# Kernel optimization log

Hardware: AMD Instinct MI355X
Metric: run time of the kernel (lower is better)

## Reference

```python
import jax, jax.numpy as jnp
import numpy as np

B, S, E = 2, 2049, 512
H, WIN = 8, 1024
D = E // H


def setup_inputs() -> dict:
    key = jax.random.key(0)
    ks = jax.random.split(key, 11)
    sc = 0.02
    return {
        "x": jax.random.normal(ks[0], (B, S, E), dtype=jnp.float32),
        "Wq": jax.random.normal(ks[1], (E, E), dtype=jnp.float32) * sc,
        "bq": jnp.zeros((E,), dtype=jnp.float32),
        "Wk": jax.random.normal(ks[2], (E, E), dtype=jnp.float32) * sc,
        "bk": jnp.zeros((E,), dtype=jnp.float32),
        "Wv": jax.random.normal(ks[3], (E, E), dtype=jnp.float32) * sc,
        "bv": jnp.zeros((E,), dtype=jnp.float32),
        "Wo": jax.random.normal(ks[4], (E, E), dtype=jnp.float32) * sc,
        "bo": jnp.zeros((E,), dtype=jnp.float32),
        "w_gate": jax.random.normal(ks[5], (2 * E,), dtype=jnp.float32) * sc,
        "b_gate": jnp.zeros((), dtype=jnp.float32),
    }


def reference(x, Wq, bq, Wk, bk, Wv, bv, Wo, bo, w_gate, b_gate):
    scale = D ** -0.5
    q_flat = x @ Wq + bq  # [B,S,E]
    k_flat = x @ Wk + bk
    v_flat = x @ Wv + bv
    q = q_flat.reshape(B, S, H, D).transpose(0, 2, 1, 3)  # [B,H,S,D]
    k = k_flat.reshape(B, S, H, D).transpose(0, 2, 1, 3)
    v = v_flat.reshape(B, S, H, D).transpose(0, 2, 1, 3)

    scores = jnp.einsum("bhqd,bhkd->bhqk", q, k) * scale  # [B,H,S,S]

    # Gaussian positional bias: -0.5*|i-j|^2/sigma^2, sigma = window/2
    pos = jnp.arange(S)
    dist = jnp.abs(pos[:, None] - pos[None, :]).astype(jnp.float32)
    sigma = WIN / 2.0
    bias = -0.5 * dist ** 2 / (sigma ** 2)  # [S,S]
    scores = scores + bias[None, None]

    # Pairwise gate: sigmoid(concat(q_i,k_j) @ w + b) == sigmoid(q_i.wq + k_j.wk + b)
    gq = q_flat @ w_gate[:E]       # [B,S]
    gk = k_flat @ w_gate[E:]       # [B,S]
    gates = jax.nn.sigmoid(gq[:, :, None] + gk[:, None, :] + b_gate)  # [B,S,S]
    scores = scores * gates[:, None]  # broadcast over heads

    local_mask = jnp.where(dist <= WIN, 0.0, -jnp.inf).astype(jnp.float32)
    scores = scores + local_mask[None, None]

    attn = jax.nn.softmax(scores, axis=-1)
    out = jnp.einsum("bhqk,bhkd->bhqd", attn, v)  # [B,H,S,D]
    out = out.transpose(0, 2, 1, 3).reshape(B, S, E)
    return out @ Wo + bo
```

## Files before the change

kernel.cpp:

```cpp
#include <hip/hip_runtime.h>
#include <cstdint>
#include <cstddef>

#define B_ 2
#define S_ 2049
#define E_ 512
#define H_ 8
#define WIN_ 1024
#define MROWS (B_*S_)
#define SP_ 2176
#define GBUFN 4104
#define BHS_ (B_*H_*S_)

typedef unsigned short ushort_t;
typedef __attribute__((ext_vector_type(8))) short bf16x8;
typedef __attribute__((ext_vector_type(4))) float f32x4;

#define MFMA16(a,b,c) __builtin_amdgcn_mfma_f32_16x16x32_bf16(a,b,c,0,0,0)

__device__ __forceinline__ ushort_t f2bf(float f) {
  unsigned int u = __float_as_uint(f);
  u += 0x7fffu + ((u >> 16) & 1u);
  return (ushort_t)(u >> 16);
}
__device__ __forceinline__ float bf2f(ushort_t h) {
  return __uint_as_float(((unsigned int)h) << 16);
}

__global__ __launch_bounds__(256) void convert_all_kernel(
    const float* __restrict__ x, const float* __restrict__ W0,
    const float* __restrict__ W1, const float* __restrict__ W2,
    const float* __restrict__ W3, ushort_t* __restrict__ xb,
    ushort_t* __restrict__ Wt_all, ushort_t* __restrict__ WoHi,
    float* __restrict__ gacc)
{
  __shared__ float tile[32][33];
  int bid = blockIdx.x;
  if (bid < 2049) {
    int idx = bid * 256 + threadIdx.x;
    float4 v = ((const float4*)x)[idx];
    ushort4 o;
    o.x = f2bf(v.x); o.y = f2bf(v.y); o.z = f2bf(v.z); o.w = f2bf(v.w);
    ((ushort4*)xb)[idx] = o;
    return;
  }
  int wid = bid - 2049;
  int z = wid >> 8, rem = wid & 255;
  if (z == 3) {
    int gz = rem * 256 + threadIdx.x;
    if (gz < 2 * GBUFN) gacc[gz] = 0.f;
  }
  const float* W = (z == 0) ? W0 : (z == 1) ? W1 : (z == 2) ? W2 : W3;
  int k0 = (rem >> 4) * 32, n0 = (rem & 15) * 32;
  int r = threadIdx.x >> 5, c = threadIdx.x & 31;
#pragma unroll
  for (int i = 0; i < 4; ++i) {
    int rr = r + i * 8;
    tile[rr][c] = W[(size_t)(k0 + rr) * E_ + n0 + c];
  }
  __syncthreads();
#pragma unroll
  for (int i = 0; i < 4; ++i) {
    int rr = r + i * 8;
    float v = tile[c][rr];
    size_t dst = (size_t)(n0 + rr) * E_ + k0 + c;
    if (z < 3) Wt_all[(size_t)z * E_ * E_ + dst] = f2bf(v);
    else       WoHi[dst] = f2bf(v);
  }
}

__global__ __launch_bounds__(256) void gemm_qkv_kernel(
    const ushort_t* __restrict__ xb, const ushort_t* __restrict__ Wt_all,
    const float* __restrict__ bq, const float* __restrict__ bk,
    const float* __restrict__ bv, const float* __restrict__ wg,
    ushort_t* __restrict__ qkb, ushort_t* __restrict__ vT,
    float* __restrict__ gacc)
{
  __shared__ __align__(16) ushort_t As[64][72];
  __shared__ __align__(16) ushort_t Bs[128][72];
  int tid = threadIdx.x;
  int lane = tid & 63, w = tid >> 6;
  int l15 = lane & 15, quad = lane >> 4;
  int wm = (w & 1) * 32, wn = (w >> 1) * 64;
  int z = blockIdx.z;
  const ushort_t* Wt = Wt_all + (size_t)z * E_ * E_;
  const float* bias = (z == 0) ? bq : (z == 1) ? bk : bv;
  int bt = blockIdx.x;
  int bg2 = bt / 33;
  int bm = (bt - bg2 * 33) * 64;
  int bn = blockIdx.y * 128;
  size_t rowbase = (size_t)bg2 * S_;

  int ar = tid >> 2, acq = (tid & 3) * 16;
  int ai = bm + ar; if (ai >= S_) ai = S_ - 1;
  const ushort_t* ap = xb + (rowbase + ai) * E_ + acq;
  int br = tid >> 1, bcq = (tid & 1) * 32;
  const ushort_t* bp = Wt + (size_t)(bn + br) * E_ + bcq;

  const f32x4 fz = {0.f, 0.f, 0.f, 0.f};
  f32x4 acc[2][4];
#pragma unroll
  for (int mt = 0; mt < 2; ++mt)
#pragma unroll
    for (int nt = 0; nt < 4; ++nt) acc[mt][nt] = fz;

  int4 pa0 = *(const int4*)ap, pa1 = *(const int4*)(ap + 8);
  int4 pb0 = *(const int4*)bp,        pb1 = *(const int4*)(bp + 8);
  int4 pb2 = *(const int4*)(bp + 16), pb3 = *(const int4*)(bp + 24);

  for (int k0 = 0; k0 < E_; k0 += 64) {
    __syncthreads();
    int kn = (k0 + 64 < E_) ? (k0 + 64) : k0;
    int4 na0 = *(const int4*)(ap + kn), na1 = *(const int4*)(ap + kn + 8);
    int4 nb0 = *(const int4*)(bp + kn),      nb1 = *(const int4*)(bp + kn + 8);
    int4 nb2 = *(const int4*)(bp + kn + 16), nb3 = *(const int4*)(bp + kn + 24);
    *(int4*)&As[ar][acq] = pa0; *(int4*)&As[ar][acq + 8] = pa1;
    *(int4*)&Bs[br][bcq] = pb0;      *(int4*)&Bs[br][bcq + 8] = pb1;
    *(int4*)&Bs[br][bcq + 16] = pb2; *(int4*)&Bs[br][bcq + 24] = pb3;
    __syncthreads();
    bf16x8 a[2][2], bfr[4][2];
#pragma unroll
    for (int mt = 0; mt < 2; ++mt) {
      a[mt][0] = *(const bf16x8*)&As[wm + mt * 16 + l15][quad * 8];
      a[mt][1] = *(const bf16x8*)&As[wm + mt * 16 + l15][32 + quad * 8];
    }
#pragma unroll
    for (int nt = 0; nt < 4; ++nt) {
      bfr[nt][0] = *(const bf16x8*)&Bs[wn + nt * 16 + l15][quad * 8];
      bfr[nt][1] = *(const bf16x8*)&Bs[wn + nt * 16 + l15][32 + quad * 8];
    }
    __builtin_amdgcn_s_setprio(1);
#pragma unroll
    for (int mt = 0; mt < 2; ++mt)
#pragma unroll
      for (int nt = 0; nt < 4; ++nt) {
        acc[mt][nt] = MFMA16(a[mt][0], bfr[nt][0], acc[mt][nt]);
        acc[mt][nt] = MFMA16(a[mt][1], bfr[nt][1], acc[mt][nt]);
      }
    __builtin_amdgcn_s_setprio(0);
    pa0 = na0; pa1 = na1; pb0 = nb0; pb1 = nb1; pb2 = nb2; pb3 = nb3;
  }

  float bb[4];
#pragma unroll
  for (int nt = 0; nt < 4; ++nt) bb[nt] = bias[bn + wn + nt * 16 + l15];

  if (z < 2) {
    ushort_t* C = qkb + (size_t)z * MROWS * E_;
#pragma unroll
    for (int mt = 0; mt < 2; ++mt)
#pragma unroll
      for (int nt = 0; nt < 4; ++nt)
#pragma unroll
        for (int r = 0; r < 4; ++r) {
          int i = bm + wm + mt * 16 + quad * 4 + r;
          if (i < S_)
            C[(rowbase + i) * E_ + bn + wn + nt * 16 + l15] = f2bf(acc[mt][nt][r] + bb[nt]);
        }
    const float* wgp = wg + (size_t)z * E_;
    float wv[4];
#pragma unroll
    for (int nt = 0; nt < 4; ++nt) wv[nt] = wgp[bn + wn + nt * 16 + l15];
    float* gp = gacc + (size_t)z * GBUFN;
#pragma unroll
    for (int mt = 0; mt < 2; ++mt)
#pragma unroll
      for (int r = 0; r < 4; ++r) {
        float s = 0.f;
#pragma unroll
        for (int nt = 0; nt < 4; ++nt) s = fmaf(acc[mt][nt][r] + bb[nt], wv[nt], s);
        s += __shfl_xor(s, 1, 16); s += __shfl_xor(s, 2, 16);
        s += __shfl_xor(s, 4, 16); s += __shfl_xor(s, 8, 16);
        int i = bm + wm + mt * 16 + quad * 4 + r;
        if (l15 == 0 && i < S_) atomicAdd(&gp[rowbase + i], s);
      }
  } else {
    ushort_t* lt = &Bs[0][0];
    int ti = tid >> 2, tc = (tid & 3) * 16;
#pragma unroll
    for (int hh = 0; hh < 2; ++hh) {
      __syncthreads();
      if ((w >> 1) == hh) {
#pragma unroll
        for (int mt = 0; mt < 2; ++mt)
#pragma unroll
          for (int nt = 0; nt < 4; ++nt) {
            int d = nt * 16 + l15;
#pragma unroll
            for (int r = 0; r < 4; ++r) {
              int il = wm + mt * 16 + quad * 4 + r;
              lt[d * 72 + il] = f2bf(acc[mt][nt][r] + bb[nt]);
            }
          }
      }
      __syncthreads();
      int hg = (bn >> 6) + hh;
      union { int4 q[2]; ushort_t u[16]; } tv;
      tv.q[0] = *(const int4*)&lt[ti * 72 + tc];
      tv.q[1] = *(const int4*)&lt[ti * 72 + tc + 8];
      size_t vrow = ((size_t)(bg2 * H_ + hg) * 64 + ti) * SP_;
#pragma unroll
      for (int c8 = 0; c8 < 2; ++c8) {
        int i2 = bm + tc + c8 * 8;
        if (i2 + 7 < S_) {
          *(int4*)&vT[vrow + i2] = tv.q[c8];
        } else {
#pragma unroll
          for (int e = 0; e < 8; ++e)
            if (i2 + e < S_) vT[vrow + i2 + e] = tv.u[c8 * 8 + e];
        }
      }
    }
  }
}

__global__ __launch_bounds__(256) void attn_kernel(
    const ushort_t* __restrict__ qb, const ushort_t* __restrict__ kb,
    const ushort_t* __restrict__ vT, const float* __restrict__ gq_raw,
    const float* __restrict__ gk_raw, const float* __restrict__ bgate,
    float* __restrict__ Opart, float* __restrict__ Lpart)
{
  __shared__ __align__(16) ushort_t Ks[64][72];
  __shared__ __align__(16) ushort_t Vt[64][72];
  __shared__ __align__(16) ushort_t Ps[4][16][72];
  __shared__ float gbs[704];

  int tid = threadIdx.x;
  int lane = tid & 63, w = tid >> 6;
  int l15 = lane & 15, quad = lane >> 4;

  int sub = blockIdx.x % 48;
  int qidx = blockIdx.x / 48;
  int off = (qidx + 1) >> 1;
  int qt = 16 + ((qidx & 1) ? -off : off);
  int bh = sub & 15, third = sub >> 4;
  int h = bh & 7, b = bh >> 3;
  int i0 = qt * 64;
  const float LOG2E = 1.44269504f;
  const float coef2 = (-0.5f / (512.f * 512.f)) * LOG2E;
  const float QSC = 0.125f * LOG2E;

  int i = i0 + w * 16 + l15;
  int ic = (i < S_) ? i : S_ - 1;
  bf16x8 qf0 = *(const bf16x8*)&qb[((size_t)(b * S_ + ic)) * E_ + h * 64 + quad * 8];
  bf16x8 qf1 = *(const bf16x8*)&qb[((size_t)(b * S_ + ic)) * E_ + h * 64 + 32 + quad * 8];
#pragma unroll
  for (int e = 0; e < 8; ++e) {
    qf0[e] = (short)f2bf(bf2f((ushort_t)qf0[e]) * QSC);
    qf1[e] = (short)f2bf(bf2f((ushort_t)qf1[e]) * QSC);
  }
  float av = __expf(-(gq_raw[b * S_ + ic] + bgate[0]));
  float fdi = (i < S_) ? (float)i : -1e5f;

  int jlo = i0 - WIN_; if (jlo < 0) jlo = 0;
  int jt_lo = jlo >> 6;
  int jhi = i0 + 63 + WIN_; if (jhi > S_ - 1) jhi = S_ - 1;
  int jt_hi = jhi >> 6;
  int L = jt_hi - jt_lo + 1;
  int n0 = (L + 2) / 3, n1 = (L + 1) / 3;
  int myLo = jt_lo + ((third == 0) ? 0 : (third == 1) ? n0 : n0 + n1);
  int cnt = (third == 0) ? n0 : (third == 1) ? n1 : L - n0 - n1;
  int myHi = myLo + cnt - 1;
  int jbase = myLo << 6;
  int nwin = cnt << 6;

  for (int tt = tid; tt < nwin; tt += 256) {
    int j = jbase + tt; int jc = (j < S_) ? j : S_ - 1;
    gbs[tt] = __expf(-gk_raw[b * S_ + jc]);
  }

  int srow = tid >> 2, scol = (tid & 3) * 16;
  const ushort_t* kb_base = kb + (size_t)b * S_ * E_ + h * 64 + scol;
  const ushort_t* vb_base = vT + ((size_t)(b * H_ + h) * 64 + srow) * SP_ + scol;

  int4 ka0, ka1, va0, va1;
  {
    int jc0 = jbase + srow; if (jc0 > S_ - 1) jc0 = S_ - 1;
    const int4* kp = (const int4*)(kb_base + (size_t)jc0 * E_);
    ka0 = kp[0]; ka1 = kp[1];
    const int4* vp = (const int4*)(vb_base + jbase);
    va0 = vp[0]; va1 = vp[1];
  }

  const f32x4 fz = {0.f, 0.f, 0.f, 0.f};
  f32x4 Ov[4] = {fz, fz, fz, fz};
  float l_run = 0.f;

  for (int jt = myLo; jt <= myHi; ++jt) {
    int j0 = jt << 6;
    __syncthreads();
    int jn = (jt < myHi) ? ((jt + 1) << 6) : j0;
    int jcn = jn + srow; if (jcn > S_ - 1) jcn = S_ - 1;
    const int4* kp = (const int4*)(kb_base + (size_t)jcn * E_);
    int4 nk0 = kp[0], nk1 = kp[1];
    const int4* vp = (const int4*)(vb_base + jn);
    int4 nv0 = vp[0], nv1 = vp[1];
    *(int4*)&Ks[srow][scol] = ka0; *(int4*)&Ks[srow][scol + 8] = ka1;
    *(int4*)&Vt[srow][scol] = va0; *(int4*)&Vt[srow][scol + 8] = va1;
    __syncthreads();

    f32x4 st[4];
    __builtin_amdgcn_s_setprio(1);
#pragma unroll
    for (int nt = 0; nt < 4; ++nt) {
      bf16x8 kf0 = *(const bf16x8*)&Ks[nt * 16 + l15][quad * 8];
      bf16x8 kf1 = *(const bf16x8*)&Ks[nt * 16 + l15][32 + quad * 8];
      f32x4 s = MFMA16(kf0, qf0, fz);
      st[nt] = MFMA16(kf1, qf1, s);
    }
    __builtin_amdgcn_s_setprio(0);

    bool full = ((j0 + 63 - i0) <= WIN_) && ((i0 + 63 - j0) <= WIN_)
                && (j0 + 63 < S_) && (i0 + 63 < S_);
    float ps = 0.f;
    float fq = fdi - (float)(j0 + quad * 4);
    if (full) {
#pragma unroll
      for (int nt = 0; nt < 4; ++nt) {
        f32x4 g4 = *(const f32x4*)&gbs[(j0 - jbase) + nt * 16 + quad * 4];
#pragma unroll
        for (int r = 0; r < 4; ++r) {
          float f = fq - (float)(nt * 16 + r);
          float gate = __builtin_amdgcn_rcpf(fmaf(av, g4[r], 1.f));
          float p = __builtin_amdgcn_exp2f(fmaf(f * f, coef2, st[nt][r]) * gate);
          st[nt][r] = p; ps += p;
        }
      }
    } else {
#pragma unroll
      for (int nt = 0; nt < 4; ++nt) {
        f32x4 g4 = *(const f32x4*)&gbs[(j0 - jbase) + nt * 16 + quad * 4];
#pragma unroll
        for (int r = 0; r < 4; ++r) {
          int j = j0 + nt * 16 + quad * 4 + r;
          float fj = (j < S_) ? (float)j : 1e5f;
          float f = fdi - fj;
          float gate = __builtin_amdgcn_rcpf(fmaf(av, g4[r], 1.f));
          float t = fmaf(f * f, coef2, st[nt][r]) * gate;
          t = (__builtin_fabsf(f) <= 1024.f) ? t : -1e30f;
          float p = __builtin_amdgcn_exp2f(t);
          st[nt][r] = p; ps += p;
        }
      }
    }
    ps += __shfl_xor(ps, 16);
    ps += __shfl_xor(ps, 32);
    l_run += ps;

#pragma unroll
    for (int nt = 0; nt < 4; ++nt) {
      uint2 pk;
      pk.x = (unsigned int)f2bf(st[nt][0]) | ((unsigned int)f2bf(st[nt][1]) << 16);
      pk.y = (unsigned int)f2bf(st[nt][2]) | ((unsigned int)f2bf(st[nt][3]) << 16);
      *(uint2*)&Ps[w][l15][nt * 16 + quad * 4] = pk;
    }
    bf16x8 p0 = *(const bf16x8*)&Ps[w][l15][quad * 8];
    bf16x8 p1 = *(const bf16x8*)&Ps[w][l15][32 + quad * 8];
    __builtin_amdgcn_s_setprio(1);
#pragma unroll
    for (int nt = 0; nt < 4; ++nt) {
      bf16x8 v0 = *(const bf16x8*)&Vt[nt * 16 + l15][quad * 8];
      bf16x8 v1 = *(const bf16x8*)&Vt[nt * 16 + l15][32 + quad * 8];
      Ov[nt] = MFMA16(p0, v0, Ov[nt]);
      Ov[nt] = MFMA16(p1, v1, Ov[nt]);
    }
    __builtin_amdgcn_s_setprio(0);
    ka0 = nk0; ka1 = nk1; va0 = nv0; va1 = nv1;
  }

  if (lane < 16) {
    int irow = i0 + w * 16 + lane;
    if (irow < S_)
      Lpart[(size_t)third * BHS_ + (size_t)(b * H_ + h) * S_ + irow] = l_run;
  }
#pragma unroll
  for (int r = 0; r < 4; ++r) {
    int irow = i0 + w * 16 + quad * 4 + r;
    if (irow < S_) {
      size_t base = ((size_t)third * BHS_ + (size_t)(b * H_ + h) * S_ + irow) * 64;
#pragma unroll
      for (int nt = 0; nt < 4; ++nt)
        Opart[base + nt * 16 + l15] = Ov[nt][r];
    }
  }
}

__global__ __launch_bounds__(256) void combine_kernel(
    const float* __restrict__ Opart, const float* __restrict__ Lpart,
    ushort_t* __restrict__ ahi, ushort_t* __restrict__ alo)
{
  int tid = threadIdx.x;
  int gi = blockIdx.x * 16 + (tid >> 4);
  int d4 = tid & 15;
  int b = gi / (H_ * S_);
  int rem = gi - b * (H_ * S_);
  int h = rem / S_;
  int i = rem - h * S_;
  size_t p0 = (size_t)(b * H_ + h) * S_ + i;
  float l = Lpart[p0] + Lpart[p0 + (size_t)BHS_] + Lpart[p0 + 2 * (size_t)BHS_];
  float inv = 1.f / l;
  const float* op = Opart + p0 * 64 + d4 * 4;
  float4 o1 = *(const float4*)op;
  float4 o2 = *(const float4*)(op + (size_t)BHS_ * 64);
  float4 o3 = *(const float4*)(op + 2 * (size_t)BHS_ * 64);
  float o[4] = {(o1.x + o2.x + o3.x) * inv, (o1.y + o2.y + o3.y) * inv,
                (o1.z + o2.z + o3.z) * inv, (o1.w + o2.w + o3.w) * inv};
  ushort4 hi, lo;
  hi.x = f2bf(o[0]); lo.x = f2bf(o[0] - bf2f(hi.x));
  hi.y = f2bf(o[1]); lo.y = f2bf(o[1] - bf2f(hi.y));
  hi.z = f2bf(o[2]); lo.z = f2bf(o[2] - bf2f(hi.z));
  hi.w = f2bf(o[3]); lo.w = f2bf(o[3] - bf2f(hi.w));
  size_t oidx = ((size_t)b * S_ + i) * E_ + h * 64 + d4 * 4;
  *(ushort4*)&ahi[oidx] = hi;
  *(ushort4*)&alo[oidx] = lo;
}

__global__ __launch_bounds__(256) void gemm_out_kernel(
    const ushort_t* __restrict__ Ahi, const ushort_t* __restrict__ Alo,
    const ushort_t* __restrict__ Whi, const float* __restrict__ bias,
    float* __restrict__ C)
{
  __shared__ __align__(16) ushort_t AsH[64][72];
  __shared__ __align__(16) ushort_t AsL[64][72];
  __shared__ __align__(16) ushort_t BsW[64][72];
  int tid = threadIdx.x;
  int lane = tid & 63, w = tid >> 6;
  int l15 = lane & 15, quad = lane >> 4;
  int wm = (w & 1) * 32, wn = (w >> 1) * 32;
  int bm = blockIdx.x * 64, bn = blockIdx.y * 64;

  int sr = tid >> 2, sc = (tid & 3) * 16;
  int am = bm + sr; if (am >= MROWS) am = MROWS - 1;
  const ushort_t* ahp = Ahi + (size_t)am * E_ + sc;
  const ushort_t* alp = Alo + (size_t)am * E_ + sc;
  const ushort_t* bp = Whi + (size_t)(bn + sr) * E_ + sc;

  const f32x4 fz = {0.f, 0.f, 0.f, 0.f};
  f32x4 acc[2][2];
#pragma unroll
  for (int mt = 0; mt < 2; ++mt)
#pragma unroll
    for (int nt = 0; nt < 2; ++nt) acc[mt][nt] = fz;

  int4 ph0 = *(const int4*)ahp, ph1 = *(const int4*)(ahp + 8);
  int4 pl0 = *(const int4*)alp, pl1 = *(const int4*)(alp + 8);
  int4 pb0 = *(const int4*)bp,  pb1 = *(const int4*)(bp + 8);

  for (int k0 = 0; k0 < E_; k0 += 64) {
    __syncthreads();
    int kn = (k0 + 64 < E_) ? (k0 + 64) : k0;
    int4 nh0 = *(const int4*)(ahp + kn), nh1 = *(const int4*)(ahp + kn + 8);
    int4 nl0 = *(const int4*)(alp + kn), nl1 = *(const int4*)(alp + kn + 8);
    int4 nb0 = *(const int4*)(bp + kn),  nb1 = *(const int4*)(bp + kn + 8);
    *(int4*)&AsH[sr][sc] = ph0; *(int4*)&AsH[sr][sc + 8] = ph1;
    *(int4*)&AsL[sr][sc] = pl0; *(int4*)&AsL[sr][sc + 8] = pl1;
    *(int4*)&BsW[sr][sc] = pb0; *(int4*)&BsW[sr][sc + 8] = pb1;
    __syncthreads();
    bf16x8 ah[2][2], al[2][2], bw[2][2];
#pragma unroll
    for (int mt = 0; mt < 2; ++mt) {
      ah[mt][0] = *(const bf16x8*)&AsH[wm + mt * 16 + l15][quad * 8];
      ah[mt][1] = *(const bf16x8*)&AsH[wm + mt * 16 + l15][32 + quad * 8];
      al[mt][0] = *(const bf16x8*)&AsL[wm + mt * 16 + l15][quad * 8];
      al[mt][1] = *(const bf16x8*)&AsL[wm + mt * 16 + l15][32 + quad * 8];
    }
#pragma unroll
    for (int nt = 0; nt < 2; ++nt) {
      bw[nt][0] = *(const bf16x8*)&BsW[wn + nt * 16 + l15][quad * 8];
      bw[nt][1] = *(const bf16x8*)&BsW[wn + nt * 16 + l15][32 + quad * 8];
    }
    __builtin_amdgcn_s_setprio(1);
#pragma unroll
    for (int mt = 0; mt < 2; ++mt)
#pragma unroll
      for (int nt = 0; nt < 2; ++nt) {
        acc[mt][nt] = MFMA16(ah[mt][0], bw[nt][0], acc[mt][nt]);
        acc[mt][nt] = MFMA16(al[mt][0], bw[nt][0], acc[mt][nt]);
        acc[mt][nt] = MFMA16(ah[mt][1], bw[nt][1], acc[mt][nt]);
        acc[mt][nt] = MFMA16(al[mt][1], bw[nt][1], acc[mt][nt]);
      }
    __builtin_amdgcn_s_setprio(0);
    ph0 = nh0; ph1 = nh1; pl0 = nl0; pl1 = nl1; pb0 = nb0; pb1 = nb1;
  }
#pragma unroll
  for (int nt = 0; nt < 2; ++nt) {
    float bb = bias[bn + wn + nt * 16 + l15];
#pragma unroll
    for (int mt = 0; mt < 2; ++mt)
#pragma unroll
      for (int r = 0; r < 4; ++r) {
        int m = bm + wm + mt * 16 + quad * 4 + r;
        if (m < MROWS)
          C[(size_t)m * E_ + bn + wn + nt * 16 + l15] = acc[mt][nt][r] + bb;
      }
  }
}

extern "C" void kernel_launch(void* const* d_in, const int* in_sizes, int n_in,
                              void* d_out, int out_size, void* d_ws, size_t ws_size,
                              hipStream_t stream) {
  const float* x  = (const float*)d_in[0];
  const float* Wq = (const float*)d_in[1];
  const float* bq = (const float*)d_in[2];
  const float* Wk = (const float*)d_in[3];
  const float* bk = (const float*)d_in[4];
  const float* Wv = (const float*)d_in[5];
  const float* bv = (const float*)d_in[6];
  const float* Wo = (const float*)d_in[7];
  const float* bo = (const float*)d_in[8];
  const float* wg = (const float*)d_in[9];
  const float* bg = (const float*)d_in[10];

  char* p = (char*)d_ws;
  ushort_t* Wt_all = (ushort_t*)p; p += (size_t)3 * E_ * E_ * 2;
  ushort_t* WoHi   = (ushort_t*)p; p += (size_t)E_ * E_ * 2;
  ushort_t* qkb    = (ushort_t*)p; p += (size_t)2 * MROWS * E_ * 2;
  ushort_t* vT     = (ushort_t*)p; p += (size_t)B_ * H_ * 64 * SP_ * 2;
  float*    gacc   = (float*)p;    p += (size_t)2 * GBUFN * 4;
  float*    Opart  = (float*)p;    p += (size_t)3 * BHS_ * 64 * 4;
  float*    Lpart  = (float*)p;    p += (size_t)3 * BHS_ * 4;
  ushort_t* xb     = (ushort_t*)Opart;
  ushort_t* aHi    = qkb;
  ushort_t* aLo    = qkb + (size_t)MROWS * E_;

  hipLaunchKernelGGL(convert_all_kernel, dim3(3073), dim3(256), 0, stream,
                     x, Wq, Wk, Wv, Wo, xb, Wt_all, WoHi, gacc);
  hipLaunchKernelGGL(gemm_qkv_kernel, dim3(66, 4, 3), dim3(256), 0, stream,
                     xb, Wt_all, bq, bk, bv, wg, qkb, vT, gacc);
  hipLaunchKernelGGL(attn_kernel, dim3(33 * 48), dim3(256), 0, stream,
                     qkb, qkb + (size_t)MROWS * E_, vT, gacc, gacc + GBUFN, bg,
                     Opart, Lpart);
  hipLaunchKernelGGL(combine_kernel, dim3(2049), dim3(256), 0, stream,
                     Opart, Lpart, aHi, aLo);
  hipLaunchKernelGGL(gemm_out_kernel, dim3(65, 8), dim3(256), 0, stream,
                     aHi, aLo, WoHi, bo, (float*)d_out);
}
```

Before: 162.9 us.

## Swizzle LDS tiles, use hardware bf16 pack, compute row sums via MFMA

Replaces the padded LDS arrays for K, V and P with unpadded 64-wide tiles using an XOR swizzle on 16-byte slots to avoid bank conflicts. The software round-to-nearest bf16 conversion is replaced by the v_cvt_pk_bf16_f32 instruction. The per-tile softmax denominator, previously a scalar sum plus cross-lane shuffles, is now accumulated by two extra MFMAs against a ones vector. The row sums are therefore taken from the bf16-rounded probabilities, which slightly changes numerics, and the extra MFMA work is added to the matrix pipe.

```diff
diff --git a/kernel.cpp b/kernel.cpp
--- a/kernel.cpp
+++ b/kernel.cpp
@@ -214,15 +214,19 @@
   }
 }
 
+__device__ __forceinline__ int swz(int row, int slot) {
+  return row * 64 + ((slot ^ (row & 7)) << 3);
+}
+
 __global__ __launch_bounds__(256) void attn_kernel(
     const ushort_t* __restrict__ qb, const ushort_t* __restrict__ kb,
     const ushort_t* __restrict__ vT, const float* __restrict__ gq_raw,
     const float* __restrict__ gk_raw, const float* __restrict__ bgate,
     float* __restrict__ Opart, float* __restrict__ Lpart)
 {
-  __shared__ __align__(16) ushort_t Ks[64][72];
-  __shared__ __align__(16) ushort_t Vt[64][72];
-  __shared__ __align__(16) ushort_t Ps[4][16][72];
+  __shared__ __align__(16) ushort_t Ks[64 * 64];
+  __shared__ __align__(16) ushort_t Vt[64 * 64];
+  __shared__ __align__(16) ushort_t Ps[4 * 16 * 64];
   __shared__ float gbs[704];
 
   int tid = threadIdx.x;
@@ -269,7 +273,9 @@
     gbs[tt] = __expf(-gk_raw[b * S_ + jc]);
   }
 
-  int srow = tid >> 2, scol = (tid & 3) * 16;
+  int srow = tid >> 2, sc4 = tid & 3;
+  int scol = sc4 * 16;
+  int wl0 = swz(srow, 2 * sc4), wl1 = swz(srow, 2 * sc4 + 1);
   const ushort_t* kb_base = kb + (size_t)b * S_ * E_ + h * 64 + scol;
   const ushort_t* vb_base = vT + ((size_t)(b * H_ + h) * 64 + srow) * SP_ + scol;
 
@@ -284,7 +290,15 @@
 
   const f32x4 fz = {0.f, 0.f, 0.f, 0.f};
   f32x4 Ov[4] = {fz, fz, fz, fz};
-  float l_run = 0.f;
+  const bf16x8 ones = {16256, 16256, 16256, 16256, 16256, 16256, 16256, 16256};
+  f32x4 Lv = fz;
+
+  int psb = w * 1024;
+  int pw[4];
+#pragma unroll
+  for (int nt = 0; nt < 4; ++nt)
+    pw[nt] = psb + l15 * 64 + (((2 * nt + (quad >> 1)) ^ (l15 & 7)) << 3) + (quad & 1) * 4;
+  int pr0 = psb + swz(l15, quad), pr1 = psb + swz(l15, 4 + quad);
 
   for (int jt = myLo; jt <= myHi; ++jt) {
     int j0 = jt << 6;
@@ -295,16 +309,17 @@
     int4 nk0 = kp[0], nk1 = kp[1];
     const int4* vp = (const int4*)(vb_base + jn);
     int4 nv0 = vp[0], nv1 = vp[1];
-    *(int4*)&Ks[srow][scol] = ka0; *(int4*)&Ks[srow][scol + 8] = ka1;
-    *(int4*)&Vt[srow][scol] = va0; *(int4*)&Vt[srow][scol + 8] = va1;
+    *(int4*)&Ks[wl0] = ka0; *(int4*)&Ks[wl1] = ka1;
+    *(int4*)&Vt[wl0] = va0; *(int4*)&Vt[wl1] = va1;
     __syncthreads();
 
     f32x4 st[4];
     __builtin_amdgcn_s_setprio(1);
 #pragma unroll
     for (int nt = 0; nt < 4; ++nt) {
-      bf16x8 kf0 = *(const bf16x8*)&Ks[nt * 16 + l15][quad * 8];
-      bf16x8 kf1 = *(const bf16x8*)&Ks[nt * 16 + l15][32 + quad * 8];
+      int Rk = nt * 16 + l15;
+      bf16x8 kf0 = *(const bf16x8*)&Ks[swz(Rk, quad)];
+      bf16x8 kf1 = *(const bf16x8*)&Ks[swz(Rk, 4 + quad)];
       f32x4 s = MFMA16(kf0, qf0, fz);
       st[nt] = MFMA16(kf1, qf1, s);
     }
@@ -312,7 +327,6 @@
 
     bool full = ((j0 + 63 - i0) <= WIN_) && ((i0 + 63 - j0) <= WIN_)
                 && (j0 + 63 < S_) && (i0 + 63 < S_);
-    float ps = 0.f;
     float fq = fdi - (float)(j0 + quad * 4);
     if (full) {
 #pragma unroll
@@ -323,7 +337,7 @@
           float f = fq - (float)(nt * 16 + r);
           float gate = __builtin_amdgcn_rcpf(fmaf(av, g4[r], 1.f));
           float p = __builtin_amdgcn_exp2f(fmaf(f * f, coef2, st[nt][r]) * gate);
-          st[nt][r] = p; ps += p;
+          st[nt][r] = p;
         }
       }
     } else {
@@ -339,39 +353,41 @@
           float t = fmaf(f * f, coef2, st[nt][r]) * gate;
           t = (__builtin_fabsf(f) <= 1024.f) ? t : -1e30f;
           float p = __builtin_amdgcn_exp2f(t);
-          st[nt][r] = p; ps += p;
+          st[nt][r] = p;
         }
       }
     }
-    ps += __shfl_xor(ps, 16);
-    ps += __shfl_xor(ps, 32);
-    l_run += ps;
 
 #pragma unroll
     for (int nt = 0; nt < 4; ++nt) {
-      uint2 pk;
-      pk.x = (unsigned int)f2bf(st[nt][0]) | ((unsigned int)f2bf(st[nt][1]) << 16);
-      pk.y = (unsigned int)f2bf(st[nt][2]) | ((unsigned int)f2bf(st[nt][3]) << 16);
-      *(uint2*)&Ps[w][l15][nt * 16 + quad * 4] = pk;
-    }
-    bf16x8 p0 = *(const bf16x8*)&Ps[w][l15][quad * 8];
-    bf16x8 p1 = *(const bf16x8*)&Ps[w][l15][32 + quad * 8];
+      unsigned int k0p, k1p;
+      asm("v_cvt_pk_bf16_f32 %0, %1, %2" : "=v"(k0p) : "v"(st[nt][0]), "v"(st[nt][1]));
+      asm("v_cvt_pk_bf16_f32 %0, %1, %2" : "=v"(k1p) : "v"(st[nt][2]), "v"(st[nt][3]));
+      uint2 pk; pk.x = k0p; pk.y = k1p;
+      *(uint2*)&Ps[pw[nt]] = pk;
+    }
+    bf16x8 p0 = *(const bf16x8*)&Ps[pr0];
+    bf16x8 p1 = *(const bf16x8*)&Ps[pr1];
     __builtin_amdgcn_s_setprio(1);
 #pragma unroll
     for (int nt = 0; nt < 4; ++nt) {
-      bf16x8 v0 = *(const bf16x8*)&Vt[nt * 16 + l15][quad * 8];
-      bf16x8 v1 = *(const bf16x8*)&Vt[nt * 16 + l15][32 + quad * 8];
+      int Rv = nt * 16 + l15;
+      bf16x8 v0 = *(const bf16x8*)&Vt[swz(Rv, quad)];
+      bf16x8 v1 = *(const bf16x8*)&Vt[swz(Rv, 4 + quad)];
       Ov[nt] = MFMA16(p0, v0, Ov[nt]);
       Ov[nt] = MFMA16(p1, v1, Ov[nt]);
     }
+    Lv = MFMA16(p0, ones, Lv);
+    Lv = MFMA16(p1, ones, Lv);
     __builtin_amdgcn_s_setprio(0);
     ka0 = nk0; ka1 = nk1; va0 = nv0; va1 = nv1;
   }
 
-  if (lane < 16) {
-    int irow = i0 + w * 16 + lane;
-    if (irow < S_)
-      Lpart[(size_t)third * BHS_ + (size_t)(b * H_ + h) * S_ + irow] = l_run;
+#pragma unroll
+  for (int r = 0; r < 4; ++r) {
+    int irow = i0 + w * 16 + quad * 4 + r;
+    if (l15 == 0 && irow < S_)
+      Lpart[(size_t)third * BHS_ + (size_t)(b * H_ + h) * S_ + irow] = Lv[r];
   }
 #pragma unroll
   for (int r = 0; r < 4; ++r) {
```

Result: no change. 159.9 us (-1.8%).
